# Kernel optimization log

Hardware: AMD Instinct MI355X
Metric: run time of the kernel (lower is better)

Reference implementation:

```python
import jax, jax.numpy as jnp
import numpy as np

D = 256; NH = 8; NL = 4; NP = 4; DH = D // NH; FF = 1024; B = 2
SHAPES = np.array([[112, 112], [56, 56], [28, 28], [14, 14]], np.int32)  # (H_l, W_l)
SIZES = (SHAPES[:, 0] * SHAPES[:, 1]).astype(np.int64)
STARTS = np.concatenate([[0], np.cumsum(SIZES)])
S = int(SIZES.sum())


def setup_inputs() -> dict:
    key = jax.random.key(0)
    ks = jax.random.split(key, 10)
    def w(k, shape, s=0.02):
        return (s * jax.random.normal(k, shape)).astype(jnp.float32)
    z = lambda *sh: jnp.zeros(sh, jnp.float32)
    return dict(
        src=w(ks[0], (B, S, D), 1.0),
        pos=w(ks[1], (B, S, D), 1.0),
        reference_points=jax.random.uniform(ks[2], (B, S, NL, 2), jnp.float32),
        spatial_shapes=jnp.asarray(SHAPES),
        level_start_index=jnp.asarray(STARTS[:-1].astype(np.int32)),
        W_off=w(ks[3], (D, NH * NL * NP * 2)), b_off=z(NH * NL * NP * 2),
        W_attn=w(ks[4], (D, NH * NL * NP)), b_attn=z(NH * NL * NP),
        W_val=w(ks[5], (D, D)), b_val=z(D),
        W_out=w(ks[6], (D, D)), b_out=z(D),
        g1=jnp.ones((D,), jnp.float32), be1=z(D),
        g2=jnp.ones((D,), jnp.float32), be2=z(D),
        W1=w(ks[7], (D, FF)), b1=z(FF),
        W2=w(ks[8], (FF, D)), b2=z(D),
    )


def _ln(x, g, b):
    m = x.mean(-1, keepdims=True)
    v = ((x - m) ** 2).mean(-1, keepdims=True)
    return (x - m) * jax.lax.rsqrt(v + 1e-5) * g + b


def _bilinear(value, Hl, Wl, loc):
    # value: [B, NH, Hl*Wl, DH]; loc: [B, S, NH, NP, 2] in [0,1] (x,y)
    # grid_sample semantics: align_corners=False, padding_mode='zeros'
    b, s = loc.shape[0], loc.shape[1]
    x = loc[..., 0] * Wl - 0.5
    y = loc[..., 1] * Hl - 0.5
    x0 = jnp.floor(x); y0 = jnp.floor(y)
    dx = x - x0; dy = y - y0
    out = jnp.zeros((b, s, NH, NP, DH), value.dtype)
    corners = ((x0, y0, (1 - dx) * (1 - dy)), (x0 + 1, y0, dx * (1 - dy)),
               (x0, y0 + 1, (1 - dx) * dy), (x0 + 1, y0 + 1, dx * dy))
    for cx, cy, wgt in corners:
        valid = (cx >= 0) & (cx < Wl) & (cy >= 0) & (cy < Hl)
        idx = (jnp.clip(cy, 0, Hl - 1) * Wl + jnp.clip(cx, 0, Wl - 1)).astype(jnp.int32)
        idx = idx.transpose(0, 2, 1, 3).reshape(b, NH, s * NP)  # [B,NH,S*NP]
        v = jnp.take_along_axis(value, idx[..., None], axis=2)   # [B,NH,S*NP,DH]
        v = v.reshape(b, NH, s, NP, DH).transpose(0, 2, 1, 3, 4)  # [B,S,NH,NP,DH]
        out = out + v * (wgt * valid.astype(value.dtype))[..., None]
    return out


def _msda(query, src, ref, W_off, b_off, W_attn, b_attn, W_val, b_val, W_out, b_out):
    b, s, _ = query.shape
    value = src @ W_val + b_val                                   # [B,S,D]
    off = (query @ W_off + b_off).reshape(b, s, NH, NL, NP, 2)
    aw = jax.nn.softmax((query @ W_attn + b_attn).reshape(b, s, NH, NL * NP), axis=-1)
    aw = aw.reshape(b, s, NH, NL, NP)
    wh = jnp.asarray(SHAPES[:, ::-1].astype(np.float32))          # [L,2] as (W,H)
    loc = ref[:, :, None, :, None, :] + off / wh[None, None, None, :, None, :]
    out = jnp.zeros((b, s, NH, DH), value.dtype)
    for l in range(NL):
        Hl, Wl = int(SHAPES[l, 0]), int(SHAPES[l, 1])
        v_l = value[:, STARTS[l]:STARTS[l + 1]].reshape(b, Hl * Wl, NH, DH)
        v_l = v_l.transpose(0, 2, 1, 3)                           # [B,NH,HW,DH]
        samp = _bilinear(v_l, Hl, Wl, loc[:, :, :, l])            # [B,S,NH,NP,DH]
        out = out + jnp.einsum('bshp,bshpd->bshd', aw[:, :, :, l], samp)
    return out.reshape(b, s, D) @ W_out + b_out


def reference(src, pos, reference_points, spatial_shapes, level_start_index,
              W_off, b_off, W_attn, b_attn, W_val, b_val, W_out, b_out,
              g1, be1, g2, be2, W1, b1, W2, b2):
    q = src + pos
    src2 = _msda(q, src, reference_points, W_off, b_off, W_attn, b_attn,
                 W_val, b_val, W_out, b_out)
    x = _ln(src + src2, g1, be1)
    f = jnp.maximum(x @ W1 + b1, 0.0) @ W2 + b2
    return _ln(x + f, g2, be2)
```

## Files before the change

kernel.cpp:

```cpp
#include <hip/hip_runtime.h>

constexpr int D_   = 256;
constexpr int NH_  = 8;
constexpr int DH_  = 32;
constexpr int NL_  = 4;
constexpr int NP_  = 4;
constexpr int FF_  = 1024;
constexpr int B_   = 2;
constexpr int S_   = 16660;
constexpr int NR_  = B_ * S_;

typedef __attribute__((ext_vector_type(8))) short bf16x8;
typedef __attribute__((ext_vector_type(4))) float f32x4;

__device__ __forceinline__ ushort f2bf(float f) {
  unsigned u = __float_as_uint(f);
  return (ushort)((u + 0x7FFFu + ((u >> 16) & 1u)) >> 16);
}

__global__ __launch_bounds__(256)
void prep_kernel(const float* __restrict__ src, const float* __restrict__ pos,
                 ushort* __restrict__ qb, ushort* __restrict__ srcb, int n4) {
  int i = blockIdx.x * 256 + threadIdx.x;
  if (i >= n4) return;
  float4 s = ((const float4*)src)[i];
  float4 p = ((const float4*)pos)[i];
  ushort4 sb = {f2bf(s.x), f2bf(s.y), f2bf(s.z), f2bf(s.w)};
  ushort4 q  = {f2bf(s.x + p.x), f2bf(s.y + p.y), f2bf(s.z + p.z), f2bf(s.w + p.w)};
  ((ushort4*)srcb)[i] = sb;
  ((ushort4*)qb)[i]   = q;
}

__global__ __launch_bounds__(256)
void cvt_weights(const float* __restrict__ Woff, const float* __restrict__ Wattn,
                 const float* __restrict__ Wval, const float* __restrict__ Wout,
                 const float* __restrict__ W1,  const float* __restrict__ W2,
                 ushort* __restrict__ out) {
  const int wi = blockIdx.y;
  const int i = blockIdx.x * 256 + threadIdx.x;
  const float* src; int K, N; size_t off;
  switch (wi) {
    case 0: src = Wval;  K = 256;  N = 256;  off = 0;      break;
    case 1: src = Woff;  K = 256;  N = 256;  off = 65536;  break;
    case 2: src = Wattn; K = 256;  N = 128;  off = 131072; break;
    case 3: src = Wout;  K = 256;  N = 256;  off = 163840; break;
    case 4: src = W1;    K = 256;  N = 1024; off = 229376; break;
    default:src = W2;    K = 1024; N = 256;  off = 491520; break;
  }
  if (i >= K * N) return;
  int k = i / N, n = i - k * N;
  out[off + (size_t)n * K + k] = f2bf(src[i]);
}

template<int MODE>
__global__ __launch_bounds__(256, 2)
void gemm_blds(const ushort* __restrict__ A, const ushort* __restrict__ Wpan,
               const float* __restrict__ bias, const float* __restrict__ bias2,
               void* __restrict__ C, void* __restrict__ C2, int M, int Ns) {
  __shared__ ushort Bs[128 * 256];
  const int tid = threadIdx.x;
  const int l = tid & 63, w = tid >> 6;
  const int l15 = l & 15, kg = l >> 4;
  const int cxor = l15 & 7;
  const int bx = blockIdx.x, by = blockIdx.y;

  const int r0 = bx * 128 + w * 16 + l15;
  const int r1 = r0 + 64;
  const int r0c = min(r0, M - 1), r1c = min(r1, M - 1);
  const ushort* a0p = A + (size_t)r0c * 256 + kg * 8;
  const ushort* a1p = A + (size_t)r1c * 256 + kg * 8;
  bf16x8 a0[8], a1[8];
#pragma unroll
  for (int kk = 0; kk < 8; ++kk) a0[kk] = *(const bf16x8*)(a0p + kk * 32);
#pragma unroll
  for (int kk = 0; kk < 8; ++kk) a1[kk] = *(const bf16x8*)(a1p + kk * 32);

  const ushort* wp = Wpan + (size_t)by * 128 * 256;
#pragma unroll
  for (int rnd = 0; rnd < 16; ++rnd) {
    int gi = rnd * 256 + tid;
    int col = gi >> 5;
    int gphys = gi & 31;
    int glog = gphys ^ (col & 7);
    __builtin_amdgcn_global_load_lds(
        (const __attribute__((address_space(1))) void*)(wp + (size_t)col * 256 + glog * 8),
        (__attribute__((address_space(3))) void*)(Bs + (size_t)(rnd * 256 + w * 64) * 8),
        16, 0, 0);
  }

  float bj[8];
#pragma unroll
  for (int ct = 0; ct < 8; ++ct) {
    int colg = by * 128 + ct * 16 + l15;
    if (MODE == 3) bj[ct] = (colg < 256) ? bias[colg] : bias2[colg - 256];
    else           bj[ct] = bias[colg];
  }

  __syncthreads();

  f32x4 acc0[8], acc1[8];
#pragma unroll
  for (int ct = 0; ct < 8; ++ct) {
    acc0[ct] = (f32x4){0.f, 0.f, 0.f, 0.f};
    acc1[ct] = (f32x4){0.f, 0.f, 0.f, 0.f};
  }
#pragma unroll
  for (int ct = 0; ct < 8; ++ct) {
    const int cb = (ct * 16 + l15) * 256;
#pragma unroll
    for (int kk = 0; kk < 8; ++kk) {
      bf16x8 b = *(const bf16x8*)(Bs + cb + (((kk * 4 + kg) ^ cxor) * 8));
      acc0[ct] = __builtin_amdgcn_mfma_f32_16x16x32_bf16(a0[kk], b, acc0[ct], 0, 0, 0);
      acc1[ct] = __builtin_amdgcn_mfma_f32_16x16x32_bf16(a1[kk], b, acc1[ct], 0, 0, 0);
    }
  }

  const int orow0 = bx * 128 + w * 16 + kg * 4;
#pragma unroll
  for (int sl = 0; sl < 2; ++sl) {
    const int rowb = orow0 + sl * 64;
#pragma unroll
    for (int ct = 0; ct < 8; ++ct) {
      const int colg = by * 128 + ct * 16 + l15;
#pragma unroll
      for (int r = 0; r < 4; ++r) {
        const int row = rowb + r;
        if (row >= M) continue;
        float v = (sl ? acc1[ct][r] : acc0[ct][r]) + bj[ct];
        if (MODE == 2) v = fmaxf(v, 0.f);
        if (MODE == 3) {
          if (colg < 256) ((float*)C )[(size_t)row * 256 + colg]       = v;
          else            ((float*)C2)[(size_t)row * 128 + (colg-256)] = v;
        } else if (MODE == 0) {
          ((float*)C)[(size_t)row * Ns + colg] = v;
        } else {
          ((ushort*)C)[(size_t)row * Ns + colg] = f2bf(v);
        }
      }
    }
  }
}

__global__ __launch_bounds__(256, 2)
void gemm_blds1024(const ushort* __restrict__ A, const ushort* __restrict__ Wpan,
                   const float* __restrict__ bias, float* __restrict__ C, int M) {
  __shared__ ushort Bs[128 * 256];
  const int tid = threadIdx.x;
  const int l = tid & 63, w = tid >> 6;
  const int l15 = l & 15, kg = l >> 4;
  const int cxor = l15 & 7;
  const int bx = blockIdx.x, by = blockIdx.y;

  const int r0 = bx * 128 + w * 16 + l15;
  const int r1 = r0 + 64;
  const int r0c = min(r0, M - 1), r1c = min(r1, M - 1);
  const ushort* a0p = A + (size_t)r0c * 1024 + kg * 8;
  const ushort* a1p = A + (size_t)r1c * 1024 + kg * 8;
  const ushort* wp = Wpan + (size_t)by * 128 * 1024;

  float bj[8];
#pragma unroll
  for (int ct = 0; ct < 8; ++ct) bj[ct] = bias[by * 128 + ct * 16 + l15];

  f32x4 acc0[8], acc1[8];
#pragma unroll
  for (int ct = 0; ct < 8; ++ct) {
    acc0[ct] = (f32x4){0.f, 0.f, 0.f, 0.f};
    acc1[ct] = (f32x4){0.f, 0.f, 0.f, 0.f};
  }

  for (int kc = 0; kc < 4; ++kc) {
#pragma unroll
    for (int rnd = 0; rnd < 16; ++rnd) {
      int gi = rnd * 256 + tid;
      int col = gi >> 5;
      int gphys = gi & 31;
      int glog = gphys ^ (col & 7);
      __builtin_amdgcn_global_load_lds(
          (const __attribute__((address_space(1))) void*)
              (wp + (size_t)col * 1024 + kc * 256 + glog * 8),
          (__attribute__((address_space(3))) void*)(Bs + (size_t)(rnd * 256 + w * 64) * 8),
          16, 0, 0);
    }
    bf16x8 a0[8], a1[8];
#pragma unroll
    for (int kk = 0; kk < 8; ++kk) a0[kk] = *(const bf16x8*)(a0p + kc * 256 + kk * 32);
#pragma unroll
    for (int kk = 0; kk < 8; ++kk) a1[kk] = *(const bf16x8*)(a1p + kc * 256 + kk * 32);

    __syncthreads();

#pragma unroll
    for (int ct = 0; ct < 8; ++ct) {
      const int cb = (ct * 16 + l15) * 256;
#pragma unroll
      for (int kk = 0; kk < 8; ++kk) {
        bf16x8 b = *(const bf16x8*)(Bs + cb + (((kk * 4 + kg) ^ cxor) * 8));
        acc0[ct] = __builtin_amdgcn_mfma_f32_16x16x32_bf16(a0[kk], b, acc0[ct], 0, 0, 0);
        acc1[ct] = __builtin_amdgcn_mfma_f32_16x16x32_bf16(a1[kk], b, acc1[ct], 0, 0, 0);
      }
    }
    __syncthreads();
  }

  const int orow0 = bx * 128 + w * 16 + kg * 4;
#pragma unroll
  for (int sl = 0; sl < 2; ++sl) {
    const int rowb = orow0 + sl * 64;
#pragma unroll
    for (int ct = 0; ct < 8; ++ct) {
      const int colg = by * 128 + ct * 16 + l15;
#pragma unroll
      for (int r = 0; r < 4; ++r) {
        const int row = rowb + r;
        if (row >= M) continue;
        C[(size_t)row * 256 + colg] = (sl ? acc1[ct][r] : acc0[ct][r]) + bj[ct];
      }
    }
  }
}

template<bool RELU, bool OUTBF16>
__global__ __launch_bounds__(256, 2)
void gemm_mfma(const ushort* __restrict__ A, const ushort* __restrict__ Wt,
               const float* __restrict__ bias, void* __restrict__ Cout,
               int M, int N, int K) {
  __shared__ ushort As[128 * 32];
  __shared__ ushort Bs[128 * 32];
  const int tid = threadIdx.x;
  const int l = tid & 63, w = tid >> 6;
  const int brow = blockIdx.x * 128, bcol = blockIdx.y * 128;
  const int rA0 = w * 32 + (l >> 2);
  const int kbl = (l & 3) ^ ((rA0 >> 1) & 3);
  const ushort* agp0 = A  + (size_t)(brow + rA0)      * K + kbl * 8;
  const ushort* agp1 = A  + (size_t)(brow + rA0 + 16) * K + kbl * 8;
  const ushort* bgp0 = Wt + (size_t)(bcol + rA0)      * K + kbl * 8;
  const ushort* bgp1 = Wt + (size_t)(bcol + rA0 + 16) * K + kbl * 8;
  ushort* asl0 = As + w * 1024; ushort* asl1 = asl0 + 512;
  ushort* bsl0 = Bs + w * 1024; ushort* bsl1 = bsl0 + 512;
  const int l15 = l & 15;
  const int kg  = l >> 4;
  const int swz = (l15 >> 1) & 3;
  const int rbase = (w & 1) * 64, cbase = (w >> 1) * 64;
  const int aoff = (rbase + l15) * 32 + ((kg ^ swz) * 8);
  const int boff = (cbase + l15) * 32 + ((kg ^ swz) * 8);
  f32x4 acc[4][4];
#pragma unroll
  for (int i = 0; i < 4; ++i)
#pragma unroll
    for (int j = 0; j < 4; ++j) acc[i][j] = (f32x4){0.f, 0.f, 0.f, 0.f};
  for (int bk = 0; bk < K; bk += 32) {
    __builtin_amdgcn_global_load_lds(
        (const __attribute__((address_space(1))) void*)(agp0 + bk),
        (__attribute__((address_space(3))) void*)asl0, 16, 0, 0);
    __builtin_amdgcn_global_load_lds(
        (const __attribute__((address_space(1))) void*)(agp1 + bk),
        (__attribute__((address_space(3))) void*)asl1, 16, 0, 0);
    __builtin_amdgcn_global_load_lds(
        (const __attribute__((address_space(1))) void*)(bgp0 + bk),
        (__attribute__((address_space(3))) void*)bsl0, 16, 0, 0);
    __builtin_amdgcn_global_load_lds(
        (const __attribute__((address_space(1))) void*)(bgp1 + bk),
        (__attribute__((address_space(3))) void*)bsl1, 16, 0, 0);
    __syncthreads();
    bf16x8 af[4], bfr[4];
#pragma unroll
    for (int i = 0; i < 4; ++i) af[i]  = *(const bf16x8*)(As + aoff + i * 512);
#pragma unroll
    for (int j = 0; j < 4; ++j) bfr[j] = *(const bf16x8*)(Bs + boff + j * 512);
#pragma unroll
    for (int i = 0; i < 4; ++i)
#pragma unroll
      for (int j = 0; j < 4; ++j)
        acc[i][j] = __builtin_amdgcn_mfma_f32_16x16x32_bf16(af[i], bfr[j], acc[i][j], 0, 0, 0);
    __syncthreads();
  }
  const int r0 = kg * 4;
#pragma unroll
  for (int j = 0; j < 4; ++j) {
    const int col = bcol + cbase + j * 16 + l15;
    const float bj = bias[col];
#pragma unroll
    for (int i = 0; i < 4; ++i) {
      const int rowb = brow + rbase + i * 16 + r0;
#pragma unroll
      for (int r = 0; r < 4; ++r) {
        const int row = rowb + r;
        if (row < M) {
          float v = acc[i][j][r] + bj;
          if (RELU) v = fmaxf(v, 0.f);
          if (OUTBF16) ((ushort*)Cout)[(size_t)row * N + col] = f2bf(v);
          else         ((float*)Cout)[(size_t)row * N + col]  = v;
        }
      }
    }
  }
}

__global__ __launch_bounds__(256)
void msda_kernel(const ushort* __restrict__ value, const float* __restrict__ offs,
                 const float* __restrict__ attn, const float* __restrict__ ref,
                 ushort* __restrict__ out) {
  __shared__ int4   descI[4 * 136];
  __shared__ float4 descW[4 * 136];
  const int t = threadIdx.x;
  const int orig = blockIdx.x;
  const int xcd = orig & 7, ii = orig >> 3;
  const int wg = (xcd < 2 ? xcd * 1042 : 2 * 1042 + (xcd - 2) * 1041) + ii;
  const int n0 = wg * 4;

  const int Hs[4] = {112, 56, 28, 14};
  const int st[4] = {0, 12544, 15680, 16464};

#pragma unroll
  for (int rep = 0; rep < 2; ++rep) {
    const int di = t + rep * 256;
    const int q = di >> 7, h = (di >> 4) & 7, lp = di & 15;
    const int lv = lp >> 2;
    const int n = n0 + q;

    float lg = attn[(size_t)n * 128 + h * 16 + lp];
    float mx = lg;
#pragma unroll
    for (int o = 8; o; o >>= 1) mx = fmaxf(mx, __shfl_xor(mx, o, 64));
    float e = __expf(lg - mx);
    float ssum = e;
#pragma unroll
    for (int o = 8; o; o >>= 1) ssum += __shfl_xor(ssum, o, 64);
    const float aw = e / ssum;

    const int Hl = Hs[lv], Wl = Hs[lv];
    const float fS = (float)Wl;
    const float refx = ref[((size_t)n * 4 + lv) * 2 + 0];
    const float refy = ref[((size_t)n * 4 + lv) * 2 + 1];
    const float ox = offs[(size_t)n * 256 + h * 32 + lp * 2 + 0];
    const float oy = offs[(size_t)n * 256 + h * 32 + lp * 2 + 1];
    float x = fmaf(refx, fS, ox) - 0.5f;
    float y = fmaf(refy, fS, oy) - 0.5f;
    float x0f = floorf(x), y0f = floorf(y);
    float dx = x - x0f, dy = y - y0f;
    int x0 = (int)x0f, y0 = (int)y0f;
    int x0c = min(max(x0, 0), Wl - 1), x1c = min(max(x0 + 1, 0), Wl - 1);
    int y0c = min(max(y0, 0), Hl - 1), y1c = min(max(y0 + 1, 0), Hl - 1);
    bool vx0 = (x0 >= 0) && (x0 < Wl), vx1 = (x0 + 1 >= 0) && (x0 + 1 < Wl);
    bool vy0 = (y0 >= 0) && (y0 < Hl), vy1 = (y0 + 1 >= 0) && (y0 + 1 < Hl);
    int4 I;
    I.x = st[lv] + y0c * Wl + x0c;
    I.y = st[lv] + y0c * Wl + x1c;
    I.z = st[lv] + y1c * Wl + x0c;
    I.w = st[lv] + y1c * Wl + x1c;
    float4 Wv;
    Wv.x = (1.f - dx) * (1.f - dy) * ((vx0 && vy0) ? aw : 0.f);
    Wv.y = dx * (1.f - dy)         * ((vx1 && vy0) ? aw : 0.f);
    Wv.z = (1.f - dx) * dy         * ((vx0 && vy1) ? aw : 0.f);
    Wv.w = dx * dy                 * ((vx1 && vy1) ? aw : 0.f);
    const int slot = q * 136 + h * 17 + lp;
    descI[slot] = I;
    descW[slot] = Wv;
  }
  __syncthreads();

  const int q = t >> 6, lane = t & 63;
  const int pth = lane >> 5;
  const int h  = (lane >> 2) & 7;
  const int cq = lane & 3;
  const int n = n0 + q;
  const int b = n / S_;
  const ushort* base = value + (size_t)b * S_ * 256 + h * 32 + cq * 8;

  float a[8] = {0.f, 0.f, 0.f, 0.f, 0.f, 0.f, 0.f, 0.f};
#pragma unroll
  for (int pt2 = 0; pt2 < 8; ++pt2) {
    const int pt = pt2 * 2 + pth;
    const int slot = q * 136 + h * 17 + pt;
    int4 I = descI[slot];
    float4 Wv = descW[slot];
    int   Ia[4] = {I.x, I.y, I.z, I.w};
    float Wa[4] = {Wv.x, Wv.y, Wv.z, Wv.w};
#pragma unroll
    for (int cr = 0; cr < 4; ++cr) {
      uint4 u = *(const uint4*)(base + (size_t)Ia[cr] * 256);
      const float wgt = Wa[cr];
      a[0] = fmaf(wgt, __uint_as_float(u.x << 16),         a[0]);
      a[1] = fmaf(wgt, __uint_as_float(u.x & 0xffff0000u), a[1]);
      a[2] = fmaf(wgt, __uint_as_float(u.y << 16),         a[2]);
      a[3] = fmaf(wgt, __uint_as_float(u.y & 0xffff0000u), a[3]);
      a[4] = fmaf(wgt, __uint_as_float(u.z << 16),         a[4]);
      a[5] = fmaf(wgt, __uint_as_float(u.z & 0xffff0000u), a[5]);
      a[6] = fmaf(wgt, __uint_as_float(u.w << 16),         a[6]);
      a[7] = fmaf(wgt, __uint_as_float(u.w & 0xffff0000u), a[7]);
    }
  }
#pragma unroll
  for (int i = 0; i < 8; ++i) a[i] += __shfl_xor(a[i], 32, 64);
  if (pth == 0) {
    uint4 o;
    o.x = ((uint)f2bf(a[1]) << 16) | f2bf(a[0]);
    o.y = ((uint)f2bf(a[3]) << 16) | f2bf(a[2]);
    o.z = ((uint)f2bf(a[5]) << 16) | f2bf(a[4]);
    o.w = ((uint)f2bf(a[7]) << 16) | f2bf(a[6]);
    *(uint4*)(out + (size_t)n * 256 + h * 32 + cq * 8) = o;
  }
}

template<bool WB>
__global__ __launch_bounds__(256)
void add_ln_kernel(const float* __restrict__ a, const float* __restrict__ r,
                   const float* __restrict__ g, const float* __restrict__ be,
                   float* __restrict__ out, ushort* __restrict__ outb, int M) {
  const int wave = threadIdx.x >> 6;
  const int lane = threadIdx.x & 63;
  const int row = blockIdx.x * 4 + wave;
  if (row >= M) return;
  const float4 av = *(const float4*)(a + (size_t)row * 256 + lane * 4);
  const float4 rv = *(const float4*)(r + (size_t)row * 256 + lane * 4);
  float4 v = {av.x + rv.x, av.y + rv.y, av.z + rv.z, av.w + rv.w};
  float s  = v.x + v.y + v.z + v.w;
  float s2 = v.x * v.x + v.y * v.y + v.z * v.z + v.w * v.w;
#pragma unroll
  for (int o = 32; o > 0; o >>= 1) {
    s  += __shfl_xor(s, o, 64);
    s2 += __shfl_xor(s2, o, 64);
  }
  const float mean = s * (1.f / 256.f);
  const float var  = s2 * (1.f / 256.f) - mean * mean;
  const float rstd = rsqrtf(var + 1e-5f);
  const float4 gv = *(const float4*)(g + lane * 4);
  const float4 bv = *(const float4*)(be + lane * 4);
  float4 o4;
  o4.x = (v.x - mean) * rstd * gv.x + bv.x;
  o4.y = (v.y - mean) * rstd * gv.y + bv.y;
  o4.z = (v.z - mean) * rstd * gv.z + bv.z;
  o4.w = (v.w - mean) * rstd * gv.w + bv.w;
  *(float4*)(out + (size_t)row * 256 + lane * 4) = o4;
  if (WB) {
    ushort4 ob = {f2bf(o4.x), f2bf(o4.y), f2bf(o4.z), f2bf(o4.w)};
    ((ushort4*)(outb + (size_t)row * 256))[lane] = ob;
  }
}

extern "C" void kernel_launch(void* const* d_in, const int* in_sizes, int n_in,
                              void* d_out, int out_size, void* d_ws, size_t ws_size,
                              hipStream_t stream) {
  const float* src    = (const float*)d_in[0];
  const float* pos    = (const float*)d_in[1];
  const float* refpts = (const float*)d_in[2];
  const float* W_off  = (const float*)d_in[5];
  const float* b_off  = (const float*)d_in[6];
  const float* W_attn = (const float*)d_in[7];
  const float* b_attn = (const float*)d_in[8];
  const float* W_val  = (const float*)d_in[9];
  const float* b_val  = (const float*)d_in[10];
  const float* W_out  = (const float*)d_in[11];
  const float* b_out  = (const float*)d_in[12];
  const float* g1     = (const float*)d_in[13];
  const float* be1    = (const float*)d_in[14];
  const float* g2     = (const float*)d_in[15];
  const float* be2    = (const float*)d_in[16];
  const float* W1     = (const float*)d_in[17];
  const float* b1     = (const float*)d_in[18];
  const float* W2     = (const float*)d_in[19];
  const float* b2     = (const float*)d_in[20];
  float* out = (float*)d_out;

  const size_t NF = (size_t)NR_ * 256;
  char* p = (char*)d_ws;
  ushort* qb   = (ushort*)p; p += NF * 2;
  ushort* srcb = (ushort*)p; p += NF * 2;
  ushort* valb = (ushort*)p; p += NF * 2;
  float*  offs = (float*) p; p += NF * 4;
  float*  attn = (float*) p; p += NF * 2;
  float*  tmp  = (float*) p; p += NF * 4;
  float*  x    = (float*) p; p += NF * 4;
  ushort* Wt   = (ushort*)p; p += 753664 * 2;
  ushort* msdab = srcb;
  ushort* xb    = qb;
  ushort* hid   = valb;
  ushort* WtVal = Wt;
  ushort* WtOA  = Wt + 65536;
  ushort* WtOut = Wt + 163840;
  ushort* Wt1   = Wt + 229376;
  ushort* Wt2   = Wt + 491520;

  dim3 blk(256);
  const int n4 = NR_ * 64;
  const int gr = (NR_ + 127) / 128;

  prep_kernel<<<(n4 + 255) / 256, blk, 0, stream>>>(src, pos, qb, srcb, n4);
  cvt_weights<<<dim3(1024, 6), blk, 0, stream>>>(W_off, W_attn, W_val, W_out, W1, W2, Wt);
  gemm_blds<1><<<dim3(gr, 2), blk, 0, stream>>>(srcb, WtVal, b_val, nullptr,
                                                valb, nullptr, NR_, 256);
  gemm_blds<3><<<dim3(gr, 3), blk, 0, stream>>>(qb, WtOA, b_off, b_attn,
                                                offs, attn, NR_, 0);
  msda_kernel<<<NR_ / 4, blk, 0, stream>>>(valb, offs, attn, refpts, msdab);
  gemm_blds<0><<<dim3(gr, 2), blk, 0, stream>>>(msdab, WtOut, b_out, nullptr,
                                                tmp, nullptr, NR_, 256);
  add_ln_kernel<true ><<<(NR_ + 3) / 4, blk, 0, stream>>>(tmp, src, g1, be1, x, xb, NR_);
  gemm_blds<2><<<dim3(gr, 8), blk, 0, stream>>>(xb, Wt1, b1, nullptr,
                                                hid, nullptr, NR_, 1024);
  gemm_blds1024<<<dim3(gr, 2), blk, 0, stream>>>(hid, Wt2, b2, tmp, NR_);
  add_ln_kernel<false><<<(NR_ + 3) / 4, blk, 0, stream>>>(tmp, x, g2, be2, out, nullptr, NR_);
}
```

Baseline: 396.7 us.

## Fuse residual-add LayerNorm into output and FFN2 GEMM epilogues

Adds a gemm_ln kernel in which each block computes all 256 output columns for 64 rows, then applies bias, residual add and LayerNorm in the epilogue. This removes the two standalone add_ln passes and the fp32 tmp round-trip through memory. The FFN1 GEMM now has each block loop over 4 weight panels, so it reuses its A rows from registers instead of reloading them in 8 separate column blocks. In exchange there are fewer, heavier blocks, the LDS weight panels are reloaded serially with extra syncs, and the per-row LN reduction runs across lanes inside the GEMM. The unused gemm_mfma kernel is deleted.

```diff
diff --git a/kernel.cpp b/kernel.cpp
--- a/kernel.cpp
+++ b/kernel.cpp
@@ -52,7 +52,7 @@
   out[off + (size_t)n * K + k] = f2bf(src[i]);
 }
 
-template<int MODE>
+template<int MODE, int NPAN>
 __global__ __launch_bounds__(256, 2)
 void gemm_blds(const ushort* __restrict__ A, const ushort* __restrict__ Wpan,
                const float* __restrict__ bias, const float* __restrict__ bias2,
@@ -75,224 +75,175 @@
 #pragma unroll
   for (int kk = 0; kk < 8; ++kk) a1[kk] = *(const bf16x8*)(a1p + kk * 32);
 
-  const ushort* wp = Wpan + (size_t)by * 128 * 256;
-#pragma unroll
-  for (int rnd = 0; rnd < 16; ++rnd) {
-    int gi = rnd * 256 + tid;
-    int col = gi >> 5;
-    int gphys = gi & 31;
-    int glog = gphys ^ (col & 7);
-    __builtin_amdgcn_global_load_lds(
-        (const __attribute__((address_space(1))) void*)(wp + (size_t)col * 256 + glog * 8),
-        (__attribute__((address_space(3))) void*)(Bs + (size_t)(rnd * 256 + w * 64) * 8),
-        16, 0, 0);
-  }
-
-  float bj[8];
-#pragma unroll
-  for (int ct = 0; ct < 8; ++ct) {
-    int colg = by * 128 + ct * 16 + l15;
-    if (MODE == 3) bj[ct] = (colg < 256) ? bias[colg] : bias2[colg - 256];
-    else           bj[ct] = bias[colg];
-  }
-
-  __syncthreads();
-
-  f32x4 acc0[8], acc1[8];
-#pragma unroll
-  for (int ct = 0; ct < 8; ++ct) {
-    acc0[ct] = (f32x4){0.f, 0.f, 0.f, 0.f};
-    acc1[ct] = (f32x4){0.f, 0.f, 0.f, 0.f};
-  }
-#pragma unroll
-  for (int ct = 0; ct < 8; ++ct) {
-    const int cb = (ct * 16 + l15) * 256;
-#pragma unroll
-    for (int kk = 0; kk < 8; ++kk) {
-      bf16x8 b = *(const bf16x8*)(Bs + cb + (((kk * 4 + kg) ^ cxor) * 8));
-      acc0[ct] = __builtin_amdgcn_mfma_f32_16x16x32_bf16(a0[kk], b, acc0[ct], 0, 0, 0);
-      acc1[ct] = __builtin_amdgcn_mfma_f32_16x16x32_bf16(a1[kk], b, acc1[ct], 0, 0, 0);
-    }
-  }
-
   const int orow0 = bx * 128 + w * 16 + kg * 4;
-#pragma unroll
-  for (int sl = 0; sl < 2; ++sl) {
-    const int rowb = orow0 + sl * 64;
+
+#pragma unroll
+  for (int pn = 0; pn < NPAN; ++pn) {
+    const int pc = by * NPAN + pn;
+    const ushort* wp = Wpan + (size_t)pc * 128 * 256;
+#pragma unroll
+    for (int rnd = 0; rnd < 16; ++rnd) {
+      int gi = rnd * 256 + tid;
+      int col = gi >> 5;
+      int glog = (gi & 31) ^ (col & 7);
+      __builtin_amdgcn_global_load_lds(
+          (const __attribute__((address_space(1))) void*)(wp + (size_t)col * 256 + glog * 8),
+          (__attribute__((address_space(3))) void*)(Bs + (size_t)(rnd * 256 + w * 64) * 8),
+          16, 0, 0);
+    }
+    float bj[8];
 #pragma unroll
     for (int ct = 0; ct < 8; ++ct) {
-      const int colg = by * 128 + ct * 16 + l15;
-#pragma unroll
-      for (int r = 0; r < 4; ++r) {
-        const int row = rowb + r;
-        if (row >= M) continue;
-        float v = (sl ? acc1[ct][r] : acc0[ct][r]) + bj[ct];
-        if (MODE == 2) v = fmaxf(v, 0.f);
-        if (MODE == 3) {
-          if (colg < 256) ((float*)C )[(size_t)row * 256 + colg]       = v;
-          else            ((float*)C2)[(size_t)row * 128 + (colg-256)] = v;
-        } else if (MODE == 0) {
-          ((float*)C)[(size_t)row * Ns + colg] = v;
-        } else {
-          ((ushort*)C)[(size_t)row * Ns + colg] = f2bf(v);
+      int colg = pc * 128 + ct * 16 + l15;
+      if (MODE == 3) bj[ct] = (colg < 256) ? bias[colg] : bias2[colg - 256];
+      else           bj[ct] = bias[colg];
+    }
+    __syncthreads();
+
+    f32x4 acc0[8], acc1[8];
+#pragma unroll
+    for (int ct = 0; ct < 8; ++ct) {
+      acc0[ct] = (f32x4){0.f, 0.f, 0.f, 0.f};
+      acc1[ct] = (f32x4){0.f, 0.f, 0.f, 0.f};
+    }
+#pragma unroll
+    for (int ct = 0; ct < 8; ++ct) {
+      const int cb = (ct * 16 + l15) * 256;
+#pragma unroll
+      for (int kk = 0; kk < 8; ++kk) {
+        bf16x8 b = *(const bf16x8*)(Bs + cb + (((kk * 4 + kg) ^ cxor) * 8));
+        acc0[ct] = __builtin_amdgcn_mfma_f32_16x16x32_bf16(a0[kk], b, acc0[ct], 0, 0, 0);
+        acc1[ct] = __builtin_amdgcn_mfma_f32_16x16x32_bf16(a1[kk], b, acc1[ct], 0, 0, 0);
+      }
+    }
+
+#pragma unroll
+    for (int sl = 0; sl < 2; ++sl) {
+      const int rowb = orow0 + sl * 64;
+#pragma unroll
+      for (int ct = 0; ct < 8; ++ct) {
+        const int colg = pc * 128 + ct * 16 + l15;
+#pragma unroll
+        for (int r = 0; r < 4; ++r) {
+          const int row = rowb + r;
+          if (row >= M) continue;
+          float v = (sl ? acc1[ct][r] : acc0[ct][r]) + bj[ct];
+          if (MODE == 2) v = fmaxf(v, 0.f);
+          if (MODE == 3) {
+            if (colg < 256) ((float*)C )[(size_t)row * 256 + colg]       = v;
+            else            ((float*)C2)[(size_t)row * 128 + (colg-256)] = v;
+          } else if (MODE == 0) {
+            ((float*)C)[(size_t)row * Ns + colg] = v;
+          } else {
+            ((ushort*)C)[(size_t)row * Ns + colg] = f2bf(v);
+          }
         }
       }
     }
-  }
-}
-
+    __syncthreads();
+  }
+}
+
+template<int KCH, bool WB>
 __global__ __launch_bounds__(256, 2)
-void gemm_blds1024(const ushort* __restrict__ A, const ushort* __restrict__ Wpan,
-                   const float* __restrict__ bias, float* __restrict__ C, int M) {
+void gemm_ln(const ushort* __restrict__ A, const ushort* __restrict__ Wpan,
+             const float* __restrict__ bias, const float* __restrict__ res,
+             const float* __restrict__ g, const float* __restrict__ be,
+             float* __restrict__ outf, ushort* __restrict__ outb, int M) {
+  constexpr int K = KCH * 256;
   __shared__ ushort Bs[128 * 256];
   const int tid = threadIdx.x;
   const int l = tid & 63, w = tid >> 6;
   const int l15 = l & 15, kg = l >> 4;
   const int cxor = l15 & 7;
-  const int bx = blockIdx.x, by = blockIdx.y;
-
-  const int r0 = bx * 128 + w * 16 + l15;
-  const int r1 = r0 + 64;
-  const int r0c = min(r0, M - 1), r1c = min(r1, M - 1);
-  const ushort* a0p = A + (size_t)r0c * 1024 + kg * 8;
-  const ushort* a1p = A + (size_t)r1c * 1024 + kg * 8;
-  const ushort* wp = Wpan + (size_t)by * 128 * 1024;
-
-  float bj[8];
-#pragma unroll
-  for (int ct = 0; ct < 8; ++ct) bj[ct] = bias[by * 128 + ct * 16 + l15];
-
-  f32x4 acc0[8], acc1[8];
-#pragma unroll
-  for (int ct = 0; ct < 8; ++ct) {
-    acc0[ct] = (f32x4){0.f, 0.f, 0.f, 0.f};
-    acc1[ct] = (f32x4){0.f, 0.f, 0.f, 0.f};
-  }
-
-  for (int kc = 0; kc < 4; ++kc) {
-#pragma unroll
-    for (int rnd = 0; rnd < 16; ++rnd) {
-      int gi = rnd * 256 + tid;
-      int col = gi >> 5;
-      int gphys = gi & 31;
-      int glog = gphys ^ (col & 7);
-      __builtin_amdgcn_global_load_lds(
-          (const __attribute__((address_space(1))) void*)
-              (wp + (size_t)col * 1024 + kc * 256 + glog * 8),
-          (__attribute__((address_space(3))) void*)(Bs + (size_t)(rnd * 256 + w * 64) * 8),
-          16, 0, 0);
-    }
-    bf16x8 a0[8], a1[8];
-#pragma unroll
-    for (int kk = 0; kk < 8; ++kk) a0[kk] = *(const bf16x8*)(a0p + kc * 256 + kk * 32);
-#pragma unroll
-    for (int kk = 0; kk < 8; ++kk) a1[kk] = *(const bf16x8*)(a1p + kc * 256 + kk * 32);
-
-    __syncthreads();
-
-#pragma unroll
-    for (int ct = 0; ct < 8; ++ct) {
-      const int cb = (ct * 16 + l15) * 256;
-#pragma unroll
-      for (int kk = 0; kk < 8; ++kk) {
-        bf16x8 b = *(const bf16x8*)(Bs + cb + (((kk * 4 + kg) ^ cxor) * 8));
-        acc0[ct] = __builtin_amdgcn_mfma_f32_16x16x32_bf16(a0[kk], b, acc0[ct], 0, 0, 0);
-        acc1[ct] = __builtin_amdgcn_mfma_f32_16x16x32_bf16(a1[kk], b, acc1[ct], 0, 0, 0);
+  const int bx = blockIdx.x;
+
+  const int r0 = bx * 64 + w * 16 + l15;
+  const int r0c = min(r0, M - 1);
+  const ushort* ap = A + (size_t)r0c * K + kg * 8;
+
+  f32x4 acc[2][8];
+#pragma unroll
+  for (int p = 0; p < 2; ++p)
+#pragma unroll
+    for (int ct = 0; ct < 8; ++ct) acc[p][ct] = (f32x4){0.f, 0.f, 0.f, 0.f};
+
+  for (int kc = 0; kc < KCH; ++kc) {
+    bf16x8 a[8];
+#pragma unroll
+    for (int kk = 0; kk < 8; ++kk) a[kk] = *(const bf16x8*)(ap + kc * 256 + kk * 32);
+#pragma unroll
+    for (int p = 0; p < 2; ++p) {
+      const ushort* wp = Wpan + (size_t)(p * 128) * K;
+#pragma unroll
+      for (int rnd = 0; rnd < 16; ++rnd) {
+        int gi = rnd * 256 + tid;
+        int col = gi >> 5;
+        int glog = (gi & 31) ^ (col & 7);
+        __builtin_amdgcn_global_load_lds(
+            (const __attribute__((address_space(1))) void*)
+                (wp + (size_t)col * K + kc * 256 + glog * 8),
+            (__attribute__((address_space(3))) void*)(Bs + (size_t)(rnd * 256 + w * 64) * 8),
+            16, 0, 0);
       }
-    }
-    __syncthreads();
-  }
-
-  const int orow0 = bx * 128 + w * 16 + kg * 4;
-#pragma unroll
-  for (int sl = 0; sl < 2; ++sl) {
-    const int rowb = orow0 + sl * 64;
-#pragma unroll
-    for (int ct = 0; ct < 8; ++ct) {
-      const int colg = by * 128 + ct * 16 + l15;
-#pragma unroll
-      for (int r = 0; r < 4; ++r) {
-        const int row = rowb + r;
-        if (row >= M) continue;
-        C[(size_t)row * 256 + colg] = (sl ? acc1[ct][r] : acc0[ct][r]) + bj[ct];
-      }
-    }
-  }
-}
-
-template<bool RELU, bool OUTBF16>
-__global__ __launch_bounds__(256, 2)
-void gemm_mfma(const ushort* __restrict__ A, const ushort* __restrict__ Wt,
-               const float* __restrict__ bias, void* __restrict__ Cout,
-               int M, int N, int K) {
-  __shared__ ushort As[128 * 32];
-  __shared__ ushort Bs[128 * 32];
-  const int tid = threadIdx.x;
-  const int l = tid & 63, w = tid >> 6;
-  const int brow = blockIdx.x * 128, bcol = blockIdx.y * 128;
-  const int rA0 = w * 32 + (l >> 2);
-  const int kbl = (l & 3) ^ ((rA0 >> 1) & 3);
-  const ushort* agp0 = A  + (size_t)(brow + rA0)      * K + kbl * 8;
-  const ushort* agp1 = A  + (size_t)(brow + rA0 + 16) * K + kbl * 8;
-  const ushort* bgp0 = Wt + (size_t)(bcol + rA0)      * K + kbl * 8;
-  const ushort* bgp1 = Wt + (size_t)(bcol + rA0 + 16) * K + kbl * 8;
-  ushort* asl0 = As + w * 1024; ushort* asl1 = asl0 + 512;
-  ushort* bsl0 = Bs + w * 1024; ushort* bsl1 = bsl0 + 512;
-  const int l15 = l & 15;
-  const int kg  = l >> 4;
-  const int swz = (l15 >> 1) & 3;
-  const int rbase = (w & 1) * 64, cbase = (w >> 1) * 64;
-  const int aoff = (rbase + l15) * 32 + ((kg ^ swz) * 8);
-  const int boff = (cbase + l15) * 32 + ((kg ^ swz) * 8);
-  f32x4 acc[4][4];
-#pragma unroll
-  for (int i = 0; i < 4; ++i)
-#pragma unroll
-    for (int j = 0; j < 4; ++j) acc[i][j] = (f32x4){0.f, 0.f, 0.f, 0.f};
-  for (int bk = 0; bk < K; bk += 32) {
-    __builtin_amdgcn_global_load_lds(
-        (const __attribute__((address_space(1))) void*)(agp0 + bk),
-        (__attribute__((address_space(3))) void*)asl0, 16, 0, 0);
-    __builtin_amdgcn_global_load_lds(
-        (const __attribute__((address_space(1))) void*)(agp1 + bk),
-        (__attribute__((address_space(3))) void*)asl1, 16, 0, 0);
-    __builtin_amdgcn_global_load_lds(
-        (const __attribute__((address_space(1))) void*)(bgp0 + bk),
-        (__attribute__((address_space(3))) void*)bsl0, 16, 0, 0);
-    __builtin_amdgcn_global_load_lds(
-        (const __attribute__((address_space(1))) void*)(bgp1 + bk),
-        (__attribute__((address_space(3))) void*)bsl1, 16, 0, 0);
-    __syncthreads();
-    bf16x8 af[4], bfr[4];
-#pragma unroll
-    for (int i = 0; i < 4; ++i) af[i]  = *(const bf16x8*)(As + aoff + i * 512);
-#pragma unroll
-    for (int j = 0; j < 4; ++j) bfr[j] = *(const bf16x8*)(Bs + boff + j * 512);
-#pragma unroll
-    for (int i = 0; i < 4; ++i)
-#pragma unroll
-      for (int j = 0; j < 4; ++j)
-        acc[i][j] = __builtin_amdgcn_mfma_f32_16x16x32_bf16(af[i], bfr[j], acc[i][j], 0, 0, 0);
-    __syncthreads();
-  }
-  const int r0 = kg * 4;
-#pragma unroll
-  for (int j = 0; j < 4; ++j) {
-    const int col = bcol + cbase + j * 16 + l15;
-    const float bj = bias[col];
-#pragma unroll
-    for (int i = 0; i < 4; ++i) {
-      const int rowb = brow + rbase + i * 16 + r0;
-#pragma unroll
-      for (int r = 0; r < 4; ++r) {
-        const int row = rowb + r;
-        if (row < M) {
-          float v = acc[i][j][r] + bj;
-          if (RELU) v = fmaxf(v, 0.f);
-          if (OUTBF16) ((ushort*)Cout)[(size_t)row * N + col] = f2bf(v);
-          else         ((float*)Cout)[(size_t)row * N + col]  = v;
+      __syncthreads();
+#pragma unroll
+      for (int ct = 0; ct < 8; ++ct) {
+        const int cb = (ct * 16 + l15) * 256;
+#pragma unroll
+        for (int kk = 0; kk < 8; ++kk) {
+          bf16x8 b = *(const bf16x8*)(Bs + cb + (((kk * 4 + kg) ^ cxor) * 8));
+          acc[p][ct] = __builtin_amdgcn_mfma_f32_16x16x32_bf16(a[kk], b, acc[p][ct], 0, 0, 0);
         }
       }
+      __syncthreads();
+    }
+  }
+
+  float gj[2][8], bej[2][8], bj[2][8];
+#pragma unroll
+  for (int p = 0; p < 2; ++p)
+#pragma unroll
+    for (int ct = 0; ct < 8; ++ct) {
+      int col = p * 128 + ct * 16 + l15;
+      gj[p][ct]  = g[col];
+      bej[p][ct] = be[col];
+      bj[p][ct]  = bias[col];
+    }
+  const int rowb = bx * 64 + w * 16 + kg * 4;
+#pragma unroll
+  for (int r = 0; r < 4; ++r) {
+    const int row = rowb + r;
+    const bool ok = row < M;
+    const int rc = min(row, M - 1);
+    float v[2][8];
+    float s = 0.f, s2 = 0.f;
+#pragma unroll
+    for (int p = 0; p < 2; ++p)
+#pragma unroll
+      for (int ct = 0; ct < 8; ++ct) {
+        int col = p * 128 + ct * 16 + l15;
+        float t = acc[p][ct][r] + bj[p][ct] + res[(size_t)rc * 256 + col];
+        v[p][ct] = t; s += t; s2 += t * t;
+      }
+#pragma unroll
+    for (int o = 1; o <= 8; o <<= 1) {
+      s  += __shfl_xor(s, o, 64);
+      s2 += __shfl_xor(s2, o, 64);
+    }
+    const float mean = s * (1.f / 256.f);
+    const float var  = s2 * (1.f / 256.f) - mean * mean;
+    const float rstd = rsqrtf(var + 1e-5f);
+    if (ok) {
+#pragma unroll
+      for (int p = 0; p < 2; ++p)
+#pragma unroll
+        for (int ct = 0; ct < 8; ++ct) {
+          int col = p * 128 + ct * 16 + l15;
+          float o = (v[p][ct] - mean) * rstd * gj[p][ct] + bej[p][ct];
+          outf[(size_t)row * 256 + col] = o;
+          if (WB) outb[(size_t)row * 256 + col] = f2bf(o);
+        }
     }
   }
 }
@@ -403,42 +354,6 @@
   }
 }
 
-template<bool WB>
-__global__ __launch_bounds__(256)
-void add_ln_kernel(const float* __restrict__ a, const float* __restrict__ r,
-                   const float* __restrict__ g, const float* __restrict__ be,
-                   float* __restrict__ out, ushort* __restrict__ outb, int M) {
-  const int wave = threadIdx.x >> 6;
-  const int lane = threadIdx.x & 63;
-  const int row = blockIdx.x * 4 + wave;
-  if (row >= M) return;
-  const float4 av = *(const float4*)(a + (size_t)row * 256 + lane * 4);
-  const float4 rv = *(const float4*)(r + (size_t)row * 256 + lane * 4);
-  float4 v = {av.x + rv.x, av.y + rv.y, av.z + rv.z, av.w + rv.w};
-  float s  = v.x + v.y + v.z + v.w;
-  float s2 = v.x * v.x + v.y * v.y + v.z * v.z + v.w * v.w;
-#pragma unroll
-  for (int o = 32; o > 0; o >>= 1) {
-    s  += __shfl_xor(s, o, 64);
-    s2 += __shfl_xor(s2, o, 64);
-  }
-  const float mean = s * (1.f / 256.f);
-  const float var  = s2 * (1.f / 256.f) - mean * mean;
-  const float rstd = rsqrtf(var + 1e-5f);
-  const float4 gv = *(const float4*)(g + lane * 4);
-  const float4 bv = *(const float4*)(be + lane * 4);
-  float4 o4;
-  o4.x = (v.x - mean) * rstd * gv.x + bv.x;
-  o4.y = (v.y - mean) * rstd * gv.y + bv.y;
-  o4.z = (v.z - mean) * rstd * gv.z + bv.z;
-  o4.w = (v.w - mean) * rstd * gv.w + bv.w;
-  *(float4*)(out + (size_t)row * 256 + lane * 4) = o4;
-  if (WB) {
-    ushort4 ob = {f2bf(o4.x), f2bf(o4.y), f2bf(o4.z), f2bf(o4.w)};
-    ((ushort4*)(outb + (size_t)row * 256))[lane] = ob;
-  }
-}
-
 extern "C" void kernel_launch(void* const* d_in, const int* in_sizes, int n_in,
                               void* d_out, int out_size, void* d_ws, size_t ws_size,
                               hipStream_t stream) {
@@ -470,7 +385,6 @@
   ushort* valb = (ushort*)p; p += NF * 2;
   float*  offs = (float*) p; p += NF * 4;
   float*  attn = (float*) p; p += NF * 2;
-  float*  tmp  = (float*) p; p += NF * 4;
   float*  x    = (float*) p; p += NF * 4;
   ushort* Wt   = (ushort*)p; p += 753664 * 2;
   ushort* msdab = srcb;
@@ -484,20 +398,20 @@
 
   dim3 blk(256);
   const int n4 = NR_ * 64;
-  const int gr = (NR_ + 127) / 128;
+  const int gr  = (NR_ + 127) / 128;
+  const int gr2 = (NR_ + 63) / 64;
 
   prep_kernel<<<(n4 + 255) / 256, blk, 0, stream>>>(src, pos, qb, srcb, n4);
   cvt_weights<<<dim3(1024, 6), blk, 0, stream>>>(W_off, W_attn, W_val, W_out, W1, W2, Wt);
-  gemm_blds<1><<<dim3(gr, 2), blk, 0, stream>>>(srcb, WtVal, b_val, nullptr,
-                                                valb, nullptr, NR_, 256);
-  gemm_blds<3><<<dim3(gr, 3), blk, 0, stream>>>(qb, WtOA, b_off, b_attn,
-                                                offs, attn, NR_, 0);
+  gemm_blds<1, 1><<<dim3(gr, 2), blk, 0, stream>>>(srcb, WtVal, b_val, nullptr,
+                                                   valb, nullptr, NR_, 256);
+  gemm_blds<3, 1><<<dim3(gr, 3), blk, 0, stream>>>(qb, WtOA, b_off, b_attn,
+                                                   offs, attn, NR_, 0);
   msda_kernel<<<NR_ / 4, blk, 0, stream>>>(valb, offs, attn, refpts, msdab);
-  gemm_blds<0><<<dim3(gr, 2), blk, 0, stream>>>(msdab, WtOut, b_out, nullptr,
-                                                tmp, nullptr, NR_, 256);
-  add_ln_kernel<true ><<<(NR_ + 3) / 4, blk, 0, stream>>>(tmp, src, g1, be1, x, xb, NR_);
-  gemm_blds<2><<<dim3(gr, 8), blk, 0, stream>>>(xb, Wt1, b1, nullptr,
-                                                hid, nullptr, NR_, 1024);
-  gemm_blds1024<<<dim3(gr, 2), blk, 0, stream>>>(hid, Wt2, b2, tmp, NR_);
-  add_ln_kernel<false><<<(NR_ + 3) / 4, blk, 0, stream>>>(tmp, x, g2, be2, out, nullptr, NR_);
-}
+  gemm_ln<1, true ><<<gr2, blk, 0, stream>>>(msdab, WtOut, b_out, src, g1, be1,
+                                             x, xb, NR_);
+  gemm_blds<2, 4><<<dim3(gr, 2), blk, 0, stream>>>(xb, Wt1, b1, nullptr,
+                                                   hid, nullptr, NR_, 1024);
+  gemm_ln<4, false><<<gr2, blk, 0, stream>>>(hid, Wt2, b2, x, g2, be2,
+                                             out, nullptr, NR_);
+}
```

After: 404.4 us. No clear change (+1.9%).
